# Kernel tuning notes

Measured on AMD Instinct MI355X. Metric: run time of the kernel, lower is better.

Reference implementation:

```python
import jax, jax.numpy as jnp
import numpy as np

B_SZ, SEQ, D_MODEL, D_STATE, EXPAND = 2, 1024, 1024, 16, 2
D_INNER = D_MODEL * EXPAND


def setup_inputs() -> dict:
    key = jax.random.key(0)
    ks = jax.random.split(key, 11)
    f32 = jnp.float32
    x = jax.random.normal(ks[0], (B_SZ, SEQ, D_MODEL), f32)
    # nn.Linear-style params (weight stored as [out, in], applied as x @ W.T + b)
    s_in = 1.0 / np.sqrt(D_MODEL)
    W_in = jax.random.uniform(ks[1], (2 * D_INNER, D_MODEL), f32, -s_in, s_in)
    b_in = jax.random.uniform(ks[2], (2 * D_INNER,), f32, -s_in, s_in)
    W_gate = jax.random.uniform(ks[3], (D_INNER, D_MODEL), f32, -s_in, s_in)
    b_gate = jax.random.uniform(ks[4], (D_INNER,), f32, -s_in, s_in)
    s_out = 1.0 / np.sqrt(D_INNER)
    W_out = jax.random.uniform(ks[5], (D_MODEL, D_INNER), f32, -s_out, s_out)
    b_out = jax.random.uniform(ks[6], (D_MODEL,), f32, -s_out, s_out)
    A_log = jax.random.uniform(ks[7], (D_INNER, D_STATE), f32, -3.0, -1.0)
    B_mat = 0.02 * jax.random.normal(ks[8], (D_INNER, D_STATE), f32)
    C_mat = 0.02 * jax.random.normal(ks[9], (D_INNER, D_STATE), f32)
    D_vec = 0.02 * jax.random.normal(ks[10], (D_INNER,), f32)
    return {"x": x, "W_in": W_in, "b_in": b_in, "W_gate": W_gate,
            "b_gate": b_gate, "W_out": W_out, "b_out": b_out,
            "A_log": A_log, "B_mat": B_mat, "C_mat": C_mat, "D_vec": D_vec}


def _selective_scan(x, delta, A_log, B_mat, C_mat, D_vec):
    # x, delta: [B, S, d_inner]
    A = -jnp.exp(A_log)            # [d_inner, d_state]
    c0 = C_mat[0]                  # [d_state]; torch code's [:,0,:,0] reads only C row 0

    def step(h, inp):
        x_t, d_t = inp             # each [B, d_inner]
        h = h * jnp.exp(A * d_t[..., None]) + (x_t * d_t)[..., None] * B_mat
        y_t = h @ c0               # [B, d_inner]
        return h, y_t

    h0 = jnp.zeros((x.shape[0], A.shape[0], A.shape[1]), x.dtype)
    xs = (jnp.moveaxis(x, 1, 0), jnp.moveaxis(delta, 1, 0))  # time-major
    _, ys = jax.lax.scan(step, h0, xs)                       # ys: [S, B, d_inner]
    y = jnp.moveaxis(ys, 0, 1)
    return y + x * D_vec


def reference(x, W_in, b_in, W_gate, b_gate, W_out, b_out, A_log, B_mat, C_mat, D_vec):
    gate = jax.nn.sigmoid(x @ W_gate.T + b_gate)            # [B,S,d_inner]
    proj = x @ W_in.T + b_in                                # [B,S,2*d_inner]
    x_proj, delta_proj = jnp.split(proj, 2, axis=-1)
    delta = jax.nn.relu(delta_proj)
    ss = _selective_scan(x_proj, delta, A_log, B_mat, C_mat, D_vec)
    return (gate * ss) @ W_out.T + b_out                    # [B,S,d_model]
```

## Files before the change

kernel.cpp:

```cpp
#include <hip/hip_runtime.h>
#include <hip/hip_bf16.h>


#define LOG2E 1.4426950408889634f

typedef float floatx4 __attribute__((ext_vector_type(4)));
typedef short short8 __attribute__((ext_vector_type(8)));

__device__ __forceinline__ float fexp2(float x) { return __builtin_amdgcn_exp2f(x); }
__device__ __forceinline__ unsigned short f2bf(float f) {
    unsigned int u = __float_as_uint(f);
    u = (u + 0x7fffu + ((u >> 16) & 1u)) >> 16;
    return (unsigned short)u;
}
__device__ __forceinline__ float bf2f(unsigned short h) {
    return __uint_as_float(((unsigned int)h) << 16);
}

#define GLDS16(gp, lp) __builtin_amdgcn_global_load_lds(                      \
    (const __attribute__((address_space(1))) void*)(gp),                      \
    (__attribute__((address_space(3))) void*)(lp), 16, 0, 0)

__global__ __launch_bounds__(256) void cast_to_bf16(
    const float* __restrict__ x, const float* __restrict__ wg,
    const float* __restrict__ wi, const float* __restrict__ wo,
    unsigned short* __restrict__ ox, unsigned short* __restrict__ owg,
    unsigned short* __restrict__ owi, unsigned short* __restrict__ owo)
{
    const size_t e = ((size_t)blockIdx.x * 256 + threadIdx.x) * 4;
    const float* src; unsigned short* dst; size_t off;
    if (e < 2097152)      { src = x;  dst = ox;  off = e; }
    else if (e < 4194304) { src = wg; dst = owg; off = e - 2097152; }
    else if (e < 8388608) { src = wi; dst = owi; off = e - 4194304; }
    else                  { src = wo; dst = owo; off = e - 8388608; }
    float4 v = *(const float4*)(src + off);
    *(ushort4*)(dst + off) = make_ushort4(f2bf(v.x), f2bf(v.y), f2bf(v.z), f2bf(v.w));
}

__global__ __launch_bounds__(256) void bias_init(
    const float* __restrict__ bias, float* __restrict__ out)
{
    const size_t e = ((size_t)blockIdx.x * 256 + threadIdx.x) * 4;
    const int col = (int)(e & 1023);
    *(float4*)(out + e) = *(const float4*)(bias + col);
}

template <int MODE, int MI>
__global__ __launch_bounds__(256, 3) void gemm_mfma(
    const unsigned short* __restrict__ A,
    const unsigned short* __restrict__ W0,
    const unsigned short* __restrict__ W1,
    const float* __restrict__ bias0, const float* __restrict__ bias1,
    unsigned short* __restrict__ gate,
    unsigned short* __restrict__ xproj, unsigned short* __restrict__ delta,
    float* __restrict__ outp, int ldk, int Ksub)
{
    constexpr int BM = MI * 32;
    constexpr int ROWA = BM / 32;
    __shared__ short As[BM * 64];
    __shared__ short Bs[128 * 64];

    const int tid = threadIdx.x;
    const int l = tid & 63, w = tid >> 6;
    const int mbase = blockIdx.y * BM;
    const int kbeg = (MODE == 2) ? blockIdx.z * Ksub : 0;
    const int kend = kbeg + Ksub;

    const unsigned short* Wp; const float* bias = nullptr; int nbase; bool isGate = false;
    if (MODE == 3) {
        const int bx = blockIdx.x;
        if (bx < 16) { Wp = W0; bias = bias0; nbase = bx * 128; isGate = true; }
        else         { Wp = W1; bias = bias1; nbase = (bx - 16) * 128; }
    } else { Wp = W0; nbase = blockIdx.x * 128; }

    const int rl = l >> 3;
    const int cs = (l & 7) ^ rl;
    size_t aoff[ROWA], boff[4];
    #pragma unroll
    for (int j = 0; j < ROWA; ++j)
        aoff[j] = (size_t)(mbase + (w * ROWA + j) * 8 + rl) * ldk + cs * 8;
    #pragma unroll
    for (int j = 0; j < 4; ++j)
        boff[j] = (size_t)(nbase + (w * 4 + j) * 8 + rl) * ldk + cs * 8;

    const int wm = (w >> 1) * (MI * 16), wn = (w & 1) * 64;
    floatx4 acc[MI][4] = {};

    for (int k0 = kbeg; k0 < kend; k0 += 64) {
        __syncthreads();
        #pragma unroll
        for (int j = 0; j < ROWA; ++j)
            GLDS16(A + aoff[j] + k0, &As[(w * ROWA + j) * 512]);
        #pragma unroll
        for (int j = 0; j < 4; ++j)
            GLDS16(Wp + boff[j] + k0, &Bs[(w * 4 + j) * 512]);
        __syncthreads();

        #pragma unroll
        for (int kk = 0; kk < 2; ++kk) {
            short8 af[MI], bfr[4];
            #pragma unroll
            for (int i = 0; i < MI; ++i) {
                const int row = wm + i * 16 + (l & 15);
                af[i] = *(const short8*)&As[row * 64 + (((kk * 4 + (l >> 4)) ^ (row & 7)) << 3)];
            }
            #pragma unroll
            for (int j = 0; j < 4; ++j) {
                const int row = wn + j * 16 + (l & 15);
                bfr[j] = *(const short8*)&Bs[row * 64 + (((kk * 4 + (l >> 4)) ^ (row & 7)) << 3)];
            }
            #pragma unroll
            for (int i = 0; i < MI; ++i)
                #pragma unroll
                for (int j = 0; j < 4; ++j)
                    acc[i][j] = __builtin_amdgcn_mfma_f32_16x16x32_bf16(af[i], bfr[j], acc[i][j], 0, 0, 0);
        }
    }

    const int crow0 = wm + (l >> 4) * 4;
    const int ccol = wn + (l & 15);
    #pragma unroll
    for (int j = 0; j < 4; ++j) {
        const int n = nbase + ccol + j * 16;
        const float bb = (MODE == 2) ? 0.0f : bias[n];
        #pragma unroll
        for (int i = 0; i < MI; ++i) {
            const int mr = mbase + crow0 + i * 16;
            #pragma unroll
            for (int r = 0; r < 4; ++r) {
                const float v = acc[i][j][r] + bb;
                const int m = mr + r;
                if (MODE == 3) {
                    if (isGate) {
                        const float s = 1.0f / (1.0f + fexp2(-v * LOG2E));
                        gate[(size_t)m * 2048 + n] = f2bf(s);
                    } else if (n < 2048) {
                        xproj[(size_t)m * 2048 + n] = f2bf(v);
                    } else {
                        delta[(size_t)m * 2048 + (n - 2048)] = f2bf(fmaxf(v, 0.0f));
                    }
                } else {
                    atomicAdd(&outp[(size_t)m * 1024 + n], v);
                }
            }
        }
    }
}

constexpr int NC = 32, CL = 32;

__global__ __launch_bounds__(256) void scan_phaseA(
    const unsigned short* __restrict__ xp, const unsigned short* __restrict__ dl,
    const float* __restrict__ A_log, const float* __restrict__ B_mat,
    float* __restrict__ Q, float* __restrict__ sumdt)
{
    const int ch = blockIdx.x * 256 + threadIdx.x;
    const int c = blockIdx.y;
    const int d = ch & 2047, b = ch >> 11;
    float Ac[16], Bv[16], h[16];
    #pragma unroll
    for (int s = 0; s < 16; ++s) {
        Ac[s] = -fexp2(A_log[d * 16 + s] * LOG2E) * LOG2E;
        Bv[s] = B_mat[d * 16 + s];
        h[s] = 0.0f;
    }
    float sd = 0.0f;
    size_t idx = ((size_t)b * 1024 + (size_t)c * CL) * 2048 + d;
    for (int t = 0; t < CL; ++t, idx += 2048) {
        const float xt = bf2f(xp[idx]), dt = bf2f(dl[idx]);
        sd += dt;
        const float xdt = xt * dt;
        #pragma unroll
        for (int s = 0; s < 16; ++s)
            h[s] = fmaf(h[s], fexp2(Ac[s] * dt), xdt * Bv[s]);
    }
    float* q = Q + ((size_t)ch * NC + c) * 16;
    #pragma unroll
    for (int s = 0; s < 16; ++s) q[s] = h[s];
    sumdt[ch * NC + c] = sd;
}

__global__ __launch_bounds__(256) void scan_phaseB(
    const float* __restrict__ A_log, const float* __restrict__ Q,
    const float* __restrict__ sumdt, float* __restrict__ hst)
{
    const int s = threadIdx.x & 15;
    const int ch = blockIdx.x * 16 + (threadIdx.x >> 4);
    const int d = ch & 2047;
    const float Ac = -fexp2(A_log[d * 16 + s] * LOG2E) * LOG2E;
    float h = 0.0f;
    const float* q = Q + (size_t)ch * NC * 16 + s;
    const float* sd = sumdt + ch * NC;
    float* hs = hst + (size_t)ch * NC * 16 + s;
    for (int c = 0; c < NC; ++c) {
        hs[c * 16] = h;
        h = fmaf(h, fexp2(Ac * sd[c]), q[c * 16]);
    }
}

__global__ __launch_bounds__(256) void scan_phaseC(
    const unsigned short* __restrict__ xp, const unsigned short* __restrict__ dl,
    const float* __restrict__ A_log, const float* __restrict__ B_mat,
    const float* __restrict__ C_mat, const float* __restrict__ D_vec,
    const unsigned short* __restrict__ gate, const float* __restrict__ hst,
    unsigned short* __restrict__ z)
{
    const int ch = blockIdx.x * 256 + threadIdx.x;
    const int c = blockIdx.y;
    const int d = ch & 2047, b = ch >> 11;
    float Ac[16], Bv[16], Cv[16], h[16];
    #pragma unroll
    for (int s = 0; s < 16; ++s) {
        Ac[s] = -fexp2(A_log[d * 16 + s] * LOG2E) * LOG2E;
        Bv[s] = B_mat[d * 16 + s];
        Cv[s] = C_mat[s];
        h[s] = hst[((size_t)ch * NC + c) * 16 + s];
    }
    const float Dv = D_vec[d];
    size_t idx = ((size_t)b * 1024 + (size_t)c * CL) * 2048 + d;
    for (int t = 0; t < CL; ++t, idx += 2048) {
        const float xt = bf2f(xp[idx]), dt = bf2f(dl[idx]);
        const float xdt = xt * dt;
        float y = 0.0f;
        #pragma unroll
        for (int s = 0; s < 16; ++s) {
            h[s] = fmaf(h[s], fexp2(Ac[s] * dt), xdt * Bv[s]);
            y = fmaf(h[s], Cv[s], y);
        }
        const float g = bf2f(gate[idx]);
        z[idx] = f2bf(g * (y + xt * Dv));
    }
}

extern "C" void kernel_launch(void* const* d_in, const int* in_sizes, int n_in,
                              void* d_out, int out_size, void* d_ws, size_t ws_size,
                              hipStream_t stream) {
    const float* x      = (const float*)d_in[0];
    const float* W_in   = (const float*)d_in[1];
    const float* b_in   = (const float*)d_in[2];
    const float* W_gate = (const float*)d_in[3];
    const float* b_gate = (const float*)d_in[4];
    const float* W_out  = (const float*)d_in[5];
    const float* b_out  = (const float*)d_in[6];
    const float* A_log  = (const float*)d_in[7];
    const float* B_mat  = (const float*)d_in[8];
    const float* C_mat  = (const float*)d_in[9];
    const float* D_vec  = (const float*)d_in[10];
    float* out = (float*)d_out;

    unsigned short* us = (unsigned short*)d_ws;
    unsigned short* gate  = us;
    unsigned short* z     = gate  + 4194304;
    unsigned short* x_bf  = z     + 4194304;
    unsigned short* wg_bf = x_bf  + 2097152;
    unsigned short* wi_bf = wg_bf + 2097152;
    unsigned short* wo_bf = wi_bf + 4194304;
    unsigned short* xproj = wo_bf + 2097152;
    unsigned short* delta = xproj + 4194304;
    float* fws = (float*)(delta + 4194304);
    float* Q     = fws;
    float* hst   = Q + 2097152;
    float* sumdt = hst + 2097152;

    dim3 blk(256);
    cast_to_bf16<<<10240, blk, 0, stream>>>(x, W_gate, W_in, W_out, x_bf, wg_bf, wi_bf, wo_bf);
    gemm_mfma<3, 4><<<dim3(48, 16), blk, 0, stream>>>(
        x_bf, wg_bf, wi_bf, b_gate, b_in, gate, xproj, delta, nullptr, 1024, 1024);
    scan_phaseA<<<dim3(16, NC), blk, 0, stream>>>(xproj, delta, A_log, B_mat, Q, sumdt);
    scan_phaseB<<<256, blk, 0, stream>>>(A_log, Q, sumdt, hst);
    scan_phaseC<<<dim3(16, NC), blk, 0, stream>>>(xproj, delta, A_log, B_mat, C_mat, D_vec, gate, hst, z);
    bias_init<<<2048, blk, 0, stream>>>(b_out, out);
    gemm_mfma<2, 2><<<dim3(8, 32, 2), blk, 0, stream>>>(
        z, wo_bf, nullptr, nullptr, nullptr, nullptr, nullptr, nullptr, out, 2048, 1024);
}
```

Baseline: 214.8 us.

## Merge cast and bias init kernels, keep xproj/delta fp32, enlarge GEMM tile

Folds the bias_init launch into the bf16 cast kernel to save one launch. Stores xproj and delta as fp32 instead of bf16, dropping conversions and improving scan accuracy, at the cost of twice the memory traffic in the scan phases. Doubles the first GEMM's M tile (MI 4 to 8, half the grid rows) and lowers the launch_bounds occupancy hint from 3 to 2 blocks per CU, which grows LDS and register use per block. The workspace layout is reordered to fit the larger fp32 buffers.

Result: no change. 212.9 us (-0.9%).

```diff
diff --git a/kernel.cpp b/kernel.cpp
--- a/kernel.cpp
+++ b/kernel.cpp
@@ -21,38 +21,38 @@
     (const __attribute__((address_space(1))) void*)(gp),                      \
     (__attribute__((address_space(3))) void*)(lp), 16, 0, 0)
 
-__global__ __launch_bounds__(256) void cast_to_bf16(
+__global__ __launch_bounds__(256) void cast_and_init(
     const float* __restrict__ x, const float* __restrict__ wg,
     const float* __restrict__ wi, const float* __restrict__ wo,
     unsigned short* __restrict__ ox, unsigned short* __restrict__ owg,
-    unsigned short* __restrict__ owi, unsigned short* __restrict__ owo)
-{
-    const size_t e = ((size_t)blockIdx.x * 256 + threadIdx.x) * 4;
-    const float* src; unsigned short* dst; size_t off;
-    if (e < 2097152)      { src = x;  dst = ox;  off = e; }
-    else if (e < 4194304) { src = wg; dst = owg; off = e - 2097152; }
-    else if (e < 8388608) { src = wi; dst = owi; off = e - 4194304; }
-    else                  { src = wo; dst = owo; off = e - 8388608; }
-    float4 v = *(const float4*)(src + off);
-    *(ushort4*)(dst + off) = make_ushort4(f2bf(v.x), f2bf(v.y), f2bf(v.z), f2bf(v.w));
-}
-
-__global__ __launch_bounds__(256) void bias_init(
-    const float* __restrict__ bias, float* __restrict__ out)
-{
-    const size_t e = ((size_t)blockIdx.x * 256 + threadIdx.x) * 4;
-    const int col = (int)(e & 1023);
-    *(float4*)(out + e) = *(const float4*)(bias + col);
+    unsigned short* __restrict__ owi, unsigned short* __restrict__ owo,
+    const float* __restrict__ b_out, float* __restrict__ out)
+{
+    const int bid = blockIdx.x;
+    if (bid < 10240) {
+        const size_t e = ((size_t)bid * 256 + threadIdx.x) * 4;
+        const float* src; unsigned short* dst; size_t off;
+        if (e < 2097152)      { src = x;  dst = ox;  off = e; }
+        else if (e < 4194304) { src = wg; dst = owg; off = e - 2097152; }
+        else if (e < 8388608) { src = wi; dst = owi; off = e - 4194304; }
+        else                  { src = wo; dst = owo; off = e - 8388608; }
+        float4 v = *(const float4*)(src + off);
+        *(ushort4*)(dst + off) = make_ushort4(f2bf(v.x), f2bf(v.y), f2bf(v.z), f2bf(v.w));
+    } else {
+        const size_t e = ((size_t)(bid - 10240) * 256 + threadIdx.x) * 4;
+        const int col = (int)(e & 1023);
+        *(float4*)(out + e) = *(const float4*)(b_out + col);
+    }
 }
 
 template <int MODE, int MI>
-__global__ __launch_bounds__(256, 3) void gemm_mfma(
+__global__ __launch_bounds__(256, 2) void gemm_mfma(
     const unsigned short* __restrict__ A,
     const unsigned short* __restrict__ W0,
     const unsigned short* __restrict__ W1,
     const float* __restrict__ bias0, const float* __restrict__ bias1,
     unsigned short* __restrict__ gate,
-    unsigned short* __restrict__ xproj, unsigned short* __restrict__ delta,
+    float* __restrict__ xproj, float* __restrict__ delta,
     float* __restrict__ outp, int ldk, int Ksub)
 {
     constexpr int BM = MI * 32;
@@ -135,9 +135,9 @@
                         const float s = 1.0f / (1.0f + fexp2(-v * LOG2E));
                         gate[(size_t)m * 2048 + n] = f2bf(s);
                     } else if (n < 2048) {
-                        xproj[(size_t)m * 2048 + n] = f2bf(v);
+                        xproj[(size_t)m * 2048 + n] = v;
                     } else {
-                        delta[(size_t)m * 2048 + (n - 2048)] = f2bf(fmaxf(v, 0.0f));
+                        delta[(size_t)m * 2048 + (n - 2048)] = fmaxf(v, 0.0f);
                     }
                 } else {
                     atomicAdd(&outp[(size_t)m * 1024 + n], v);
@@ -150,7 +150,7 @@
 constexpr int NC = 32, CL = 32;
 
 __global__ __launch_bounds__(256) void scan_phaseA(
-    const unsigned short* __restrict__ xp, const unsigned short* __restrict__ dl,
+    const float* __restrict__ xp, const float* __restrict__ dl,
     const float* __restrict__ A_log, const float* __restrict__ B_mat,
     float* __restrict__ Q, float* __restrict__ sumdt)
 {
@@ -167,7 +167,7 @@
     float sd = 0.0f;
     size_t idx = ((size_t)b * 1024 + (size_t)c * CL) * 2048 + d;
     for (int t = 0; t < CL; ++t, idx += 2048) {
-        const float xt = bf2f(xp[idx]), dt = bf2f(dl[idx]);
+        const float xt = xp[idx], dt = dl[idx];
         sd += dt;
         const float xdt = xt * dt;
         #pragma unroll
@@ -199,7 +199,7 @@
 }
 
 __global__ __launch_bounds__(256) void scan_phaseC(
-    const unsigned short* __restrict__ xp, const unsigned short* __restrict__ dl,
+    const float* __restrict__ xp, const float* __restrict__ dl,
     const float* __restrict__ A_log, const float* __restrict__ B_mat,
     const float* __restrict__ C_mat, const float* __restrict__ D_vec,
     const unsigned short* __restrict__ gate, const float* __restrict__ hst,
@@ -219,7 +219,7 @@
     const float Dv = D_vec[d];
     size_t idx = ((size_t)b * 1024 + (size_t)c * CL) * 2048 + d;
     for (int t = 0; t < CL; ++t, idx += 2048) {
-        const float xt = bf2f(xp[idx]), dt = bf2f(dl[idx]);
+        const float xt = xp[idx], dt = dl[idx];
         const float xdt = xt * dt;
         float y = 0.0f;
         #pragma unroll
@@ -248,28 +248,28 @@
     const float* D_vec  = (const float*)d_in[10];
     float* out = (float*)d_out;
 
-    unsigned short* us = (unsigned short*)d_ws;
+    float* fws = (float*)d_ws;
+    float* xproj = fws;
+    float* delta = xproj + 4194304;
+    float* Q     = delta + 4194304;
+    float* hst   = Q + 2097152;
+    float* sumdt = hst + 2097152;
+    unsigned short* us = (unsigned short*)(sumdt + 131072);
     unsigned short* gate  = us;
     unsigned short* z     = gate  + 4194304;
     unsigned short* x_bf  = z     + 4194304;
     unsigned short* wg_bf = x_bf  + 2097152;
     unsigned short* wi_bf = wg_bf + 2097152;
     unsigned short* wo_bf = wi_bf + 4194304;
-    unsigned short* xproj = wo_bf + 2097152;
-    unsigned short* delta = xproj + 4194304;
-    float* fws = (float*)(delta + 4194304);
-    float* Q     = fws;
-    float* hst   = Q + 2097152;
-    float* sumdt = hst + 2097152;
 
     dim3 blk(256);
-    cast_to_bf16<<<10240, blk, 0, stream>>>(x, W_gate, W_in, W_out, x_bf, wg_bf, wi_bf, wo_bf);
-    gemm_mfma<3, 4><<<dim3(48, 16), blk, 0, stream>>>(
+    cast_and_init<<<12288, blk, 0, stream>>>(x, W_gate, W_in, W_out,
+                                             x_bf, wg_bf, wi_bf, wo_bf, b_out, out);
+    gemm_mfma<3, 8><<<dim3(48, 8), blk, 0, stream>>>(
         x_bf, wg_bf, wi_bf, b_gate, b_in, gate, xproj, delta, nullptr, 1024, 1024);
     scan_phaseA<<<dim3(16, NC), blk, 0, stream>>>(xproj, delta, A_log, B_mat, Q, sumdt);
     scan_phaseB<<<256, blk, 0, stream>>>(A_log, Q, sumdt, hst);
     scan_phaseC<<<dim3(16, NC), blk, 0, stream>>>(xproj, delta, A_log, B_mat, C_mat, D_vec, gate, hst, z);
-    bias_init<<<2048, blk, 0, stream>>>(b_out, out);
     gemm_mfma<2, 2><<<dim3(8, 32, 2), blk, 0, stream>>>(
         z, wo_bf, nullptr, nullptr, nullptr, nullptr, nullptr, nullptr, out, 2048, 1024);
 }
```
